# Kernel optimization log

Hardware: AMD Instinct MI355X
Metric: run time of the kernel (lower is better)

The kernel has to match this reference:

```python
import jax, jax.numpy as jnp
import numpy as np

N_NODES = 50000
D_IN = 64
HID = 64
OUT = 64
NEG_SLOPE = 0.2


def setup_inputs() -> dict:
    key = jax.random.key(0)
    ks = jax.random.split(key, 16)
    s = 1.0 / np.sqrt(D_IN)
    inp = {
        "x": jax.random.normal(ks[0], (N_NODES, D_IN), dtype=jnp.float32),
        "edge_index": jax.random.randint(ks[1], (2, 1200000), 0, N_NODES, dtype=jnp.int64),
        # conv1 (GATConv, heads=1): separate src/dst projections + attention vectors + bias
        "W1_src": jax.random.uniform(ks[2], (D_IN, HID), jnp.float32, -s, s),
        "W1_dst": jax.random.uniform(ks[3], (D_IN, HID), jnp.float32, -s, s),
        "att1_src": jax.random.uniform(ks[4], (HID,), jnp.float32, -s, s),
        "att1_dst": jax.random.uniform(ks[5], (HID,), jnp.float32, -s, s),
        "b1": jnp.zeros((HID,), jnp.float32),
        # lin1 residual
        "Wl1": jax.random.uniform(ks[6], (D_IN, HID), jnp.float32, -s, s),
        "bl1": jnp.zeros((HID,), jnp.float32),
        # conv2
        "W2_src": jax.random.uniform(ks[7], (HID, OUT), jnp.float32, -s, s),
        "W2_dst": jax.random.uniform(ks[8], (HID, OUT), jnp.float32, -s, s),
        "att2_src": jax.random.uniform(ks[9], (OUT,), jnp.float32, -s, s),
        "att2_dst": jax.random.uniform(ks[10], (OUT,), jnp.float32, -s, s),
        "b2": jnp.zeros((OUT,), jnp.float32),
        # lin2 residual
        "Wl2": jax.random.uniform(ks[11], (HID, OUT), jnp.float32, -s, s),
        "bl2": jnp.zeros((OUT,), jnp.float32),
    }
    return inp


def _gat_conv(x, W_src, W_dst, att_src, att_dst, bias, src, dst, n_nodes):
    # project nodes: [N, C]
    h_src = x @ W_src
    h_dst = x @ W_dst
    # per-node attention logits: [N]
    a_src = h_src @ att_src
    a_dst = h_dst @ att_dst
    # per-edge score, leaky relu (slope 0.2)
    e = a_src[src] + a_dst[dst]  # [E]
    e = jnp.where(e >= 0, e, NEG_SLOPE * e)
    # segment softmax over incoming edges of each dst node
    seg_max = jax.lax.stop_gradient(
        jax.ops.segment_max(e, dst, num_segments=n_nodes))  # [N]
    w = jnp.exp(e - seg_max[dst])  # [E]
    seg_sum = jax.ops.segment_sum(w, dst, num_segments=n_nodes)  # [N]
    alpha = w / seg_sum[dst]  # [E]
    # weighted scatter-add of gathered src features
    msg = h_src[src] * alpha[:, None]  # [E, C]
    out = jax.ops.segment_sum(msg, dst, num_segments=n_nodes)  # [N, C]
    return out + bias


def reference(x, edge_index, W1_src, W1_dst, att1_src, att1_dst, b1, Wl1, bl1,
              W2_src, W2_dst, att2_src, att2_dst, b2, Wl2, bl2):
    src, dst = edge_index[0], edge_index[1]
    n = x.shape[0]
    h = _gat_conv(x, W1_src, W1_dst, att1_src, att1_dst, b1, src, dst, n)
    h = jax.nn.relu(h + x @ Wl1 + bl1)
    o = _gat_conv(h, W2_src, W2_dst, att2_src, att2_dst, b2, src, dst, n)
    o = jax.nn.relu(o + h @ Wl2 + bl2)
    return o
```

## Files before the change

kernel.cpp:

```cpp
#include <hip/hip_runtime.h>
#include <hip/hip_fp16.h>

#define NEG 0.2f
#define BSHIFT 9
#define BNODES 512
#define ECAP 14336

typedef _Float16 half8_t __attribute__((ext_vector_type(8)));
typedef float   floatx4_t __attribute__((ext_vector_type(4)));
typedef float   floatx2_t __attribute__((ext_vector_type(2)));

__device__ __forceinline__ void agg16(
    int beg, int end, float ad, int l,
    const int* __restrict__ ssrc, const float* __restrict__ asrc,
    const unsigned* __restrict__ h4,
    float& a0, float& a1, float& a2, float& a3, float& sumw) {
    a0 = a1 = a2 = a3 = sumw = 0.f;
    int e = beg;
    for (; e + 3 < end; e += 4) {
        int s0 = ssrc[e], s1 = ssrc[e + 1], s2 = ssrc[e + 2], s3 = ssrc[e + 3];
        float x0 = asrc[s0] + ad, x1 = asrc[s1] + ad;
        float x2 = asrc[s2] + ad, x3 = asrc[s3] + ad;
        unsigned v0 = h4[(size_t)s0 * 16 + l];
        unsigned v1 = h4[(size_t)s1 * 16 + l];
        unsigned v2 = h4[(size_t)s2 * 16 + l];
        unsigned v3 = h4[(size_t)s3 * 16 + l];
        x0 = (x0 >= 0.f) ? x0 : NEG * x0;
        x1 = (x1 >= 0.f) ? x1 : NEG * x1;
        x2 = (x2 >= 0.f) ? x2 : NEG * x2;
        x3 = (x3 >= 0.f) ? x3 : NEG * x3;
        float w0 = __expf(x0), w1 = __expf(x1), w2 = __expf(x2), w3 = __expf(x3);
        floatx2_t f00 = __builtin_amdgcn_cvt_pk_f32_fp8(v0, false);
        floatx2_t f01 = __builtin_amdgcn_cvt_pk_f32_fp8(v0, true);
        floatx2_t f10 = __builtin_amdgcn_cvt_pk_f32_fp8(v1, false);
        floatx2_t f11 = __builtin_amdgcn_cvt_pk_f32_fp8(v1, true);
        floatx2_t f20 = __builtin_amdgcn_cvt_pk_f32_fp8(v2, false);
        floatx2_t f21 = __builtin_amdgcn_cvt_pk_f32_fp8(v2, true);
        floatx2_t f30 = __builtin_amdgcn_cvt_pk_f32_fp8(v3, false);
        floatx2_t f31 = __builtin_amdgcn_cvt_pk_f32_fp8(v3, true);
        sumw += (w0 + w1) + (w2 + w3);
        a0 += w0 * f00.x + w1 * f10.x + w2 * f20.x + w3 * f30.x;
        a1 += w0 * f00.y + w1 * f10.y + w2 * f20.y + w3 * f30.y;
        a2 += w0 * f01.x + w1 * f11.x + w2 * f21.x + w3 * f31.x;
        a3 += w0 * f01.y + w1 * f11.y + w2 * f21.y + w3 * f31.y;
    }
    for (; e < end; ++e) {
        int s = ssrc[e];
        float x = asrc[s] + ad;
        unsigned v = h4[(size_t)s * 16 + l];
        x = (x >= 0.f) ? x : NEG * x;
        float w = __expf(x);
        floatx2_t f0 = __builtin_amdgcn_cvt_pk_f32_fp8(v, false);
        floatx2_t f1 = __builtin_amdgcn_cvt_pk_f32_fp8(v, true);
        sumw += w;
        a0 += w * f0.x; a1 += w * f0.y;
        a2 += w * f1.x; a3 += w * f1.y;
    }
}

__global__ __launch_bounds__(256) void bin_prep(
    const int* __restrict__ src, const int* __restrict__ dst,
    int* __restrict__ gcur, unsigned* __restrict__ binned, int E, int K,
    const float* __restrict__ W1s, const float* __restrict__ a1s,
    const float* __restrict__ W1d, const float* __restrict__ a1d,
    const float* __restrict__ W2s, const float* __restrict__ a2s,
    const float* __restrict__ W2d, const float* __restrict__ a2d,
    const float* __restrict__ Wl1, const float* __restrict__ Wl2,
    __half* __restrict__ wf) {
    int t = threadIdx.x;
    if (blockIdx.x == gridDim.x - 1) {
        __shared__ float vsm[256];
        {
            int g = t >> 6, k = t & 63;
            const float* W = (g == 0) ? W1s : (g == 1) ? W1d : (g == 2) ? W2s : W2d;
            const float* a = (g == 0) ? a1s : (g == 1) ? a1d : (g == 2) ? a2s : a2d;
            float s = 0.f;
            #pragma unroll 8
            for (int j = 0; j < 64; ++j) s += W[k * 64 + j] * a[j];
            vsm[t] = s;
        }
        __syncthreads();
        __half* wS1 = wf;
        __half* wL1 = wf + 4096;
        __half* wV1 = wf + 8192;
        __half* wS2 = wf + 9216;
        __half* wL2 = wf + 13312;
        __half* wV2 = wf + 17408;
        for (int e = t; e < 4096; e += 256) {
            int j = e & 7, ln = (e >> 3) & 63, tile = e >> 9;
            int nt = tile >> 1, kt = tile & 1;
            int kk = kt * 32 + ((ln >> 4) << 3) + j;
            int nn = (nt << 4) + (ln & 15);
            int wi = kk * 64 + nn;
            wS1[e] = __float2half(W1s[wi]);
            wL1[e] = __float2half(Wl1[wi]);
            wS2[e] = __float2half(W2s[wi]);
            wL2[e] = __float2half(Wl2[wi]);
        }
        for (int e = t; e < 1024; e += 256) {
            int j = e & 7, ln = (e >> 3) & 63, kt = e >> 9;
            int kk = kt * 32 + ((ln >> 4) << 3) + j;
            int nn = ln & 15;
            float v1 = (nn == 0) ? vsm[kk] : (nn == 1) ? vsm[64 + kk] : 0.f;
            float v2 = (nn == 0) ? vsm[128 + kk] : (nn == 1) ? vsm[192 + kk] : 0.f;
            wV1[e] = __float2half(v1);
            wV2[e] = __float2half(v2);
        }
        return;
    }
    __shared__ int h[128], cbase[128], cur[128];
    if (t < 128) h[t] = 0;
    __syncthreads();
    int base = blockIdx.x * 2048;
    #pragma unroll
    for (int i = 0; i < 8; ++i) {
        int idx = base + i * 256 + t;
        if (idx < E) atomicAdd(&h[dst[idx] >> BSHIFT], 1);
    }
    __syncthreads();
    if (t < K) {
        cbase[t] = t * ECAP + (h[t] ? atomicAdd(&gcur[t], h[t]) : 0);
        cur[t] = 0;
    }
    __syncthreads();
    #pragma unroll
    for (int i = 0; i < 8; ++i) {
        int idx = base + i * 256 + t;
        if (idx < E) {
            int d = dst[idx], s = src[idx];
            int b = d >> BSHIFT;
            int pos = cbase[b] + atomicAdd(&cur[b], 1);
            binned[pos] = ((unsigned)s << BSHIFT) | (unsigned)(d & (BNODES - 1));
        }
    }
}

__device__ __forceinline__ void mfma_tile(
    int tid, int row0, int rows,
    _Float16* xh, float* xf,
    const __half* wsF, const __half* wlF, const __half* wvF,
    const float* __restrict__ bconv, const float* __restrict__ blin,
    unsigned* __restrict__ hsrc8, float* __restrict__ base_out,
    float* __restrict__ asrc, float* __restrict__ adst) {
    int w = tid >> 6, lane = tid & 63, m = lane & 15, q = lane >> 4;
    half8_t a0 = *(const half8_t*)&xh[(w * 16 + m) * 72 + q * 8];
    half8_t a1 = *(const half8_t*)&xh[(w * 16 + m) * 72 + 32 + q * 8];
    const half8_t* bS = (const half8_t*)(const void*)wsF;
    const half8_t* bL = (const half8_t*)(const void*)wlF;
    const half8_t* bV = (const half8_t*)(const void*)wvF;
    floatx4_t z = {0.f, 0.f, 0.f, 0.f};
    floatx4_t cs[4], cl[4], cv;
    #pragma unroll
    for (int nt = 0; nt < 4; ++nt) {
        cs[nt] = __builtin_amdgcn_mfma_f32_16x16x32_f16(a0, bS[(nt * 2 + 0) * 64 + lane], z, 0, 0, 0);
        cs[nt] = __builtin_amdgcn_mfma_f32_16x16x32_f16(a1, bS[(nt * 2 + 1) * 64 + lane], cs[nt], 0, 0, 0);
        cl[nt] = __builtin_amdgcn_mfma_f32_16x16x32_f16(a0, bL[(nt * 2 + 0) * 64 + lane], z, 0, 0, 0);
        cl[nt] = __builtin_amdgcn_mfma_f32_16x16x32_f16(a1, bL[(nt * 2 + 1) * 64 + lane], cl[nt], 0, 0, 0);
    }
    cv = __builtin_amdgcn_mfma_f32_16x16x32_f16(a0, bV[lane], z, 0, 0, 0);
    cv = __builtin_amdgcn_mfma_f32_16x16x32_f16(a1, bV[64 + lane], cv, 0, 0, 0);
    __syncthreads();
    #pragma unroll
    for (int nt = 0; nt < 4; ++nt)
        #pragma unroll
        for (int r = 0; r < 4; ++r)
            xf[(w * 16 + q * 4 + r) * 68 + nt * 16 + m] = cs[nt][r];
    __syncthreads();
    #pragma unroll
    for (int i = 0; i < 2; ++i) {
        int u = tid + i * 256;
        int r = u >> 3, c8 = (u & 7) * 8;
        if (r < rows) {
            float4 v0 = *(const float4*)&xf[r * 68 + c8];
            float4 v1 = *(const float4*)&xf[r * 68 + c8 + 4];
            int lo = __builtin_amdgcn_cvt_pk_fp8_f32(v0.x, v0.y, 0, false);
            lo = __builtin_amdgcn_cvt_pk_fp8_f32(v0.z, v0.w, lo, true);
            int hi = __builtin_amdgcn_cvt_pk_fp8_f32(v1.x, v1.y, 0, false);
            hi = __builtin_amdgcn_cvt_pk_fp8_f32(v1.z, v1.w, hi, true);
            uint2 pk; pk.x = (unsigned)lo; pk.y = (unsigned)hi;
            *(uint2*)&hsrc8[(size_t)(row0 + r) * 16 + (u & 7) * 2] = pk;
        }
    }
    __syncthreads();
    float bb[4];
    bb[0] = bconv[m] + blin[m];
    bb[1] = bconv[16 + m] + blin[16 + m];
    bb[2] = bconv[32 + m] + blin[32 + m];
    bb[3] = bconv[48 + m] + blin[48 + m];
    #pragma unroll
    for (int nt = 0; nt < 4; ++nt)
        #pragma unroll
        for (int r = 0; r < 4; ++r)
            xf[(w * 16 + q * 4 + r) * 68 + nt * 16 + m] = cl[nt][r] + bb[nt];
    __syncthreads();
    #pragma unroll
    for (int i = 0; i < 4; ++i) {
        int u = tid + i * 256;
        int r = u >> 4, c4 = (u & 15) * 4;
        if (r < rows)
            *(float4*)&base_out[(size_t)(row0 + r) * 64 + c4] = *(const float4*)&xf[r * 68 + c4];
    }
    int rb = w * 16 + q * 4;
    if (m == 0) {
        #pragma unroll
        for (int r = 0; r < 4; ++r)
            if (rb + r < rows) asrc[row0 + rb + r] = cv[r];
    } else if (m == 1) {
        #pragma unroll
        for (int r = 0; r < 4; ++r)
            if (rb + r < rows) adst[row0 + rb + r] = cv[r];
    }
}

__global__ __launch_bounds__(256) void csr_gemm(
    const unsigned* __restrict__ binned, int* __restrict__ ssrc,
    const int* __restrict__ gcur, int* __restrict__ rowbeg, int* __restrict__ rowend,
    const float* __restrict__ x, const __half* __restrict__ wsF,
    const __half* __restrict__ wlF, const __half* __restrict__ wvF,
    const float* __restrict__ bconv, const float* __restrict__ blin,
    unsigned* __restrict__ hsrc8, float* __restrict__ base_out,
    float* __restrict__ asrc, float* __restrict__ adst, int N, int K) {
    __shared__ union {
        struct { int lh[512]; int ps[256]; } c;
        _Float16 xh[64 * 72];
        float    xf[64 * 68];
    } sm;
    int tid = threadIdx.x;
    int blk = blockIdx.x;

    if (blk < K) {
        int base = blk * ECAP;
        int cnt = min(gcur[blk], ECAP);
        sm.c.lh[tid] = 0; sm.c.lh[tid + 256] = 0;
        __syncthreads();
        for (int i = tid; i < cnt; i += 256)
            atomicAdd(&sm.c.lh[binned[base + i] & (BNODES - 1)], 1);
        __syncthreads();
        int a0 = sm.c.lh[2 * tid], a1 = sm.c.lh[2 * tid + 1];
        sm.c.ps[tid] = a0 + a1;
        __syncthreads();
        for (int off = 1; off < 256; off <<= 1) {
            int v = (tid >= off) ? sm.c.ps[tid - off] : 0;
            __syncthreads();
            sm.c.ps[tid] += v;
            __syncthreads();
        }
        int exc = sm.c.ps[tid] - (a0 + a1);
        int node0 = blk * BNODES + 2 * tid, node1 = node0 + 1;
        if (node0 < N) { rowbeg[node0] = base + exc;      rowend[node0] = base + exc + a0; }
        if (node1 < N) { rowbeg[node1] = base + exc + a0; rowend[node1] = base + exc + a0 + a1; }
        __syncthreads();
        sm.c.lh[2 * tid] = exc; sm.c.lh[2 * tid + 1] = exc + a0;
        __syncthreads();
        for (int i = tid; i < cnt; i += 256) {
            unsigned e = binned[base + i];
            int pos = atomicAdd(&sm.c.lh[e & (BNODES - 1)], 1);
            ssrc[base + pos] = (int)(e >> BSHIFT);
        }
        return;
    }

    int gb = blk - K;
    int row0 = gb * 64;
    int rows = min(64, N - row0);
    #pragma unroll
    for (int i = 0; i < 4; ++i) {
        int u = tid + i * 256;
        int r = u >> 4, c4 = (u & 15) * 4;
        if (r < rows) {
            float4 v = *(const float4*)&x[(size_t)(row0 + r) * 64 + c4];
            *(__half2*)&sm.xh[r * 72 + c4]     = __floats2half2_rn(v.x, v.y);
            *(__half2*)&sm.xh[r * 72 + c4 + 2] = __floats2half2_rn(v.z, v.w);
        }
    }
    __syncthreads();
    mfma_tile(tid, row0, rows, sm.xh, sm.xf, wsF, wlF, wvF,
              bconv, blin, hsrc8, base_out, asrc, adst);
}

__global__ __launch_bounds__(256) void node_gemm2(
    const __half* __restrict__ xh_in, const __half* __restrict__ wsF,
    const __half* __restrict__ wlF, const __half* __restrict__ wvF,
    const float* __restrict__ bconv, const float* __restrict__ blin,
    unsigned* __restrict__ hsrc8, float* __restrict__ base_out,
    float* __restrict__ asrc, float* __restrict__ adst, int N) {
    __shared__ union {
        _Float16 xh[64 * 72];
        float    xf[64 * 68];
    } sm;
    int tid = threadIdx.x;
    int row0 = blockIdx.x * 64;
    int rows = min(64, N - row0);
    #pragma unroll
    for (int i = 0; i < 2; ++i) {
        int u = tid + i * 256;
        int r = u >> 3, c8 = (u & 7) * 8;
        if (r < rows)
            *(float4*)&sm.xh[r * 72 + c8] =
                *(const float4*)&xh_in[(size_t)(row0 + r) * 64 + c8];
    }
    __syncthreads();
    mfma_tile(tid, row0, rows, sm.xh, sm.xf, wsF, wlF, wvF,
              bconv, blin, hsrc8, base_out, asrc, adst);
}

__global__ __launch_bounds__(256) void gat_aggregate_h(
    const int* __restrict__ rowbeg, const int* __restrict__ rowend,
    const int* __restrict__ ssrc,
    const float* __restrict__ asrc, const float* __restrict__ adst,
    const unsigned* __restrict__ h4, const float* __restrict__ base,
    __half2* __restrict__ out, int N) {
    int d = blockIdx.x * 16 + (threadIdx.x >> 4);
    int l = threadIdx.x & 15;
    if (d >= N) return;
    float a0, a1, a2, a3, sw;
    agg16(rowbeg[d], rowend[d], adst[d], l, ssrc, asrc, h4,
          a0, a1, a2, a3, sw);
    float4 b4 = *(const float4*)&base[(size_t)d * 64 + 4 * l];
    float invw = (sw > 0.f) ? 1.f / sw : 0.f;
    float2 pk;
    ((__half2*)&pk)[0] = __floats2half2_rn(fmaxf(b4.x + a0 * invw, 0.f),
                                           fmaxf(b4.y + a1 * invw, 0.f));
    ((__half2*)&pk)[1] = __floats2half2_rn(fmaxf(b4.z + a2 * invw, 0.f),
                                           fmaxf(b4.w + a3 * invw, 0.f));
    *(float2*)&out[(size_t)d * 32 + 2 * l] = pk;
}

__global__ __launch_bounds__(256) void gat_aggregate_f(
    const int* __restrict__ rowbeg, const int* __restrict__ rowend,
    const int* __restrict__ ssrc,
    const float* __restrict__ asrc, const float* __restrict__ adst,
    const unsigned* __restrict__ h4, const float* __restrict__ base,
    float* __restrict__ out, int N) {
    int d = blockIdx.x * 16 + (threadIdx.x >> 4);
    int l = threadIdx.x & 15;
    if (d >= N) return;
    float a0, a1, a2, a3, sw;
    agg16(rowbeg[d], rowend[d], adst[d], l, ssrc, asrc, h4,
          a0, a1, a2, a3, sw);
    float4 b4 = *(const float4*)&base[(size_t)d * 64 + 4 * l];
    float invw = (sw > 0.f) ? 1.f / sw : 0.f;
    float4 o;
    o.x = fmaxf(b4.x + a0 * invw, 0.f);
    o.y = fmaxf(b4.y + a1 * invw, 0.f);
    o.z = fmaxf(b4.z + a2 * invw, 0.f);
    o.w = fmaxf(b4.w + a3 * invw, 0.f);
    *(float4*)&out[(size_t)d * 64 + 4 * l] = o;
}

extern "C" void kernel_launch(void* const* d_in, const int* in_sizes, int n_in,
                              void* d_out, int out_size, void* d_ws, size_t ws_size,
                              hipStream_t stream) {
    const float* x    = (const float*)d_in[0];
    const int*   ei   = (const int*)d_in[1];
    const float* W1s  = (const float*)d_in[2];
    const float* W1d  = (const float*)d_in[3];
    const float* a1s  = (const float*)d_in[4];
    const float* a1d  = (const float*)d_in[5];
    const float* b1   = (const float*)d_in[6];
    const float* Wl1  = (const float*)d_in[7];
    const float* bl1  = (const float*)d_in[8];
    const float* W2s  = (const float*)d_in[9];
    const float* W2d  = (const float*)d_in[10];
    const float* a2s  = (const float*)d_in[11];
    const float* a2d  = (const float*)d_in[12];
    const float* b2   = (const float*)d_in[13];
    const float* Wl2  = (const float*)d_in[14];
    const float* bl2  = (const float*)d_in[15];

    const int N = in_sizes[0] / 64;
    const int E = in_sizes[1] / 2;
    const int* src = ei;
    const int* dst = ei + E;
    const int K = (N + BNODES - 1) >> BSHIFT;

    float* ws = (float*)d_ws;
    size_t o = 0;
    unsigned* hsrc8 = (unsigned*)(ws + o); o += (size_t)N * 16;
    __half2* hmidH  = (__half2*)(ws + o); o += (size_t)N * 32;
    float* base   = ws + o; o += (size_t)N * 64;
    float* asrc   = ws + o; o += N;
    float* adst   = ws + o; o += N;
    __half* wf    = (__half*)(ws + o); o += 9216;
    int* rowbeg = (int*)(ws + o); o += N;
    int* rowend = (int*)(ws + o); o += N;
    int* gcur   = (int*)(ws + o); o += 128;
    unsigned* binned = (unsigned*)(ws + o); o += (size_t)K * ECAP;
    int* ssrc   = (int*)(ws + o); o += (size_t)K * ECAP;

    const __half* wS1 = wf;
    const __half* wL1 = wf + 4096;
    const __half* wV1 = wf + 8192;
    const __half* wS2 = wf + 9216;
    const __half* wL2 = wf + 13312;
    const __half* wV2 = wf + 17408;

    const int EB = (E + 2047) / 2048;
    const int GB = (N + 63) / 64;
    const int AB = (N + 15) / 16;

    (void)hipMemsetAsync(gcur, 0, 128 * sizeof(int), stream);
    bin_prep<<<EB + 1, 256, 0, stream>>>(src, dst, gcur, binned, E, K,
                                         W1s, a1s, W1d, a1d, W2s, a2s, W2d, a2d,
                                         Wl1, Wl2, wf);

    csr_gemm<<<K + GB, 256, 0, stream>>>(
        binned, ssrc, gcur, rowbeg, rowend,
        x, wS1, wL1, wV1, b1, bl1,
        hsrc8, base, asrc, adst, N, K);

    gat_aggregate_h<<<AB, 256, 0, stream>>>(
        rowbeg, rowend, ssrc, asrc, adst, hsrc8, base, hmidH, N);

    node_gemm2<<<GB, 256, 0, stream>>>((const __half*)hmidH, wS2, wL2, wV2,
                                       b2, bl2, hsrc8, base, asrc, adst, N);

    gat_aggregate_f<<<AB, 256, 0, stream>>>(
        rowbeg, rowend, ssrc, asrc, adst, hsrc8, base,
        (float*)d_out, N);
}
```

Before: 207.1 us.

## Fuse layer-1 aggregation into the layer-2 node GEMM kernel

Merges the first-layer GAT aggregation and the second-layer projection GEMM into one kernel. Each 64-row block aggregates its rows straight into shared-memory fp16 tiles and then runs the MFMA tile. This removes one kernel launch and the global round trip of the fp16 hidden activations. To avoid read/write hazards across blocks, the workspace buffers are split into separate layer-1 and layer-2 copies. The cost is fewer blocks (N/64) doing the irregular gather work, each with a longer serial aggregation phase before the GEMM, which may hurt latency hiding.

```diff
diff --git a/kernel.cpp b/kernel.cpp
--- a/kernel.cpp
+++ b/kernel.cpp
@@ -278,12 +278,16 @@
               bconv, blin, hsrc8, base_out, asrc, adst);
 }
 
-__global__ __launch_bounds__(256) void node_gemm2(
-    const __half* __restrict__ xh_in, const __half* __restrict__ wsF,
-    const __half* __restrict__ wlF, const __half* __restrict__ wvF,
+__global__ __launch_bounds__(256) void agg_gemm2(
+    const int* __restrict__ rowbeg, const int* __restrict__ rowend,
+    const int* __restrict__ ssrc,
+    const float* __restrict__ asrc1, const float* __restrict__ adst1,
+    const unsigned* __restrict__ h4_1, const float* __restrict__ base1,
+    const __half* __restrict__ wsF, const __half* __restrict__ wlF,
+    const __half* __restrict__ wvF,
     const float* __restrict__ bconv, const float* __restrict__ blin,
-    unsigned* __restrict__ hsrc8, float* __restrict__ base_out,
-    float* __restrict__ asrc, float* __restrict__ adst, int N) {
+    unsigned* __restrict__ hsrc8_2, float* __restrict__ base2,
+    float* __restrict__ asrc2, float* __restrict__ adst2, int N) {
     __shared__ union {
         _Float16 xh[64 * 72];
         float    xf[64 * 68];
@@ -291,39 +295,28 @@
     int tid = threadIdx.x;
     int row0 = blockIdx.x * 64;
     int rows = min(64, N - row0);
-    #pragma unroll
-    for (int i = 0; i < 2; ++i) {
-        int u = tid + i * 256;
-        int r = u >> 3, c8 = (u & 7) * 8;
-        if (r < rows)
-            *(float4*)&sm.xh[r * 72 + c8] =
-                *(const float4*)&xh_in[(size_t)(row0 + r) * 64 + c8];
+    int g = tid >> 4, l = tid & 15;
+    #pragma unroll
+    for (int r = 0; r < 4; ++r) {
+        int rl = r * 16 + g;
+        int d = row0 + rl;
+        if (rl < rows) {
+            float a0, a1, a2, a3, sw;
+            agg16(rowbeg[d], rowend[d], adst1[d], l, ssrc, asrc1, h4_1,
+                  a0, a1, a2, a3, sw);
+            float4 b4 = *(const float4*)&base1[(size_t)d * 64 + 4 * l];
+            float invw = (sw > 0.f) ? 1.f / sw : 0.f;
+            __half2 p0 = __floats2half2_rn(fmaxf(b4.x + a0 * invw, 0.f),
+                                           fmaxf(b4.y + a1 * invw, 0.f));
+            __half2 p1 = __floats2half2_rn(fmaxf(b4.z + a2 * invw, 0.f),
+                                           fmaxf(b4.w + a3 * invw, 0.f));
+            *(__half2*)&sm.xh[rl * 72 + 4 * l]     = p0;
+            *(__half2*)&sm.xh[rl * 72 + 4 * l + 2] = p1;
+        }
     }
     __syncthreads();
     mfma_tile(tid, row0, rows, sm.xh, sm.xf, wsF, wlF, wvF,
-              bconv, blin, hsrc8, base_out, asrc, adst);
-}
-
-__global__ __launch_bounds__(256) void gat_aggregate_h(
-    const int* __restrict__ rowbeg, const int* __restrict__ rowend,
-    const int* __restrict__ ssrc,
-    const float* __restrict__ asrc, const float* __restrict__ adst,
-    const unsigned* __restrict__ h4, const float* __restrict__ base,
-    __half2* __restrict__ out, int N) {
-    int d = blockIdx.x * 16 + (threadIdx.x >> 4);
-    int l = threadIdx.x & 15;
-    if (d >= N) return;
-    float a0, a1, a2, a3, sw;
-    agg16(rowbeg[d], rowend[d], adst[d], l, ssrc, asrc, h4,
-          a0, a1, a2, a3, sw);
-    float4 b4 = *(const float4*)&base[(size_t)d * 64 + 4 * l];
-    float invw = (sw > 0.f) ? 1.f / sw : 0.f;
-    float2 pk;
-    ((__half2*)&pk)[0] = __floats2half2_rn(fmaxf(b4.x + a0 * invw, 0.f),
-                                           fmaxf(b4.y + a1 * invw, 0.f));
-    ((__half2*)&pk)[1] = __floats2half2_rn(fmaxf(b4.z + a2 * invw, 0.f),
-                                           fmaxf(b4.w + a3 * invw, 0.f));
-    *(float2*)&out[(size_t)d * 32 + 2 * l] = pk;
+              bconv, blin, hsrc8_2, base2, asrc2, adst2);
 }
 
 __global__ __launch_bounds__(256) void gat_aggregate_f(
@@ -376,11 +369,14 @@
 
     float* ws = (float*)d_ws;
     size_t o = 0;
-    unsigned* hsrc8 = (unsigned*)(ws + o); o += (size_t)N * 16;
-    __half2* hmidH  = (__half2*)(ws + o); o += (size_t)N * 32;
-    float* base   = ws + o; o += (size_t)N * 64;
-    float* asrc   = ws + o; o += N;
-    float* adst   = ws + o; o += N;
+    unsigned* hsrc8_1 = (unsigned*)(ws + o); o += (size_t)N * 16;
+    unsigned* hsrc8_2 = (unsigned*)(ws + o); o += (size_t)N * 16;
+    float* base1  = ws + o; o += (size_t)N * 64;
+    float* base2  = ws + o; o += (size_t)N * 64;
+    float* asrc1  = ws + o; o += N;
+    float* adst1  = ws + o; o += N;
+    float* asrc2  = ws + o; o += N;
+    float* adst2  = ws + o; o += N;
     __half* wf    = (__half*)(ws + o); o += 9216;
     int* rowbeg = (int*)(ws + o); o += N;
     int* rowend = (int*)(ws + o); o += N;
@@ -407,15 +403,14 @@
     csr_gemm<<<K + GB, 256, 0, stream>>>(
         binned, ssrc, gcur, rowbeg, rowend,
         x, wS1, wL1, wV1, b1, bl1,
-        hsrc8, base, asrc, adst, N, K);
-
-    gat_aggregate_h<<<AB, 256, 0, stream>>>(
-        rowbeg, rowend, ssrc, asrc, adst, hsrc8, base, hmidH, N);
-
-    node_gemm2<<<GB, 256, 0, stream>>>((const __half*)hmidH, wS2, wL2, wV2,
-                                       b2, bl2, hsrc8, base, asrc, adst, N);
+        hsrc8_1, base1, asrc1, adst1, N, K);
+
+    agg_gemm2<<<GB, 256, 0, stream>>>(
+        rowbeg, rowend, ssrc, asrc1, adst1, hsrc8_1, base1,
+        wS2, wL2, wV2, b2, bl2,
+        hsrc8_2, base2, asrc2, adst2, N);
 
     gat_aggregate_f<<<AB, 256, 0, stream>>>(
-        rowbeg, rowend, ssrc, asrc, adst, hsrc8, base,
+        rowbeg, rowend, ssrc, asrc2, adst2, hsrc8_2, base2,
         (float*)d_out, N);
 }
```

Result: no change. 209.4 us (+1.1%).
